# Optimization experiments

Measured on AMD Instinct MI355X. Metric: run time of the kernel, lower is better.

The kernel has to match this reference:

```python
import jax, jax.numpy as jnp
import numpy as np

INF = 1e38  # matches torch module's INF = 1e+38


def setup_inputs() -> dict:
    key = jax.random.key(0)
    k1, k2, k3 = jax.random.split(key, 3)
    n_len, batch, dim = 2048, 4, 512
    # scale query so QK^T logits don't fully saturate the softmax
    query = jax.random.normal(k1, (n_len, batch, dim), dtype=jnp.float32) * 0.05
    W_in = jax.random.normal(k2, (dim, dim), dtype=jnp.float32) * (1.0 / np.sqrt(dim))
    W_out = jax.random.normal(k3, (dim, 2 * dim), dtype=jnp.float32) * (1.0 / np.sqrt(2 * dim))
    return {"query": query, "W_in": W_in, "W_out": W_out}


def reference(query, W_in, W_out):
    # query: [n_len, batch, dim]; torch .t() swaps first two dims -> [batch, n_len, dim]
    q = jnp.transpose(query, (1, 0, 2))
    b, n, d = q.shape
    # attention_type == 'general': linear_in (no bias), y = x @ W^T
    q = jnp.einsum('bnd,ed->bne', q, W_in)
    # scores: [b, n, n]
    scores = jnp.einsum('bnd,bmd->bnm', q, q)
    # mask = triu(ones) INCLUDING diagonal -> set to -INF (row 0 fully masked)
    mask = jnp.triu(jnp.ones((n, n), dtype=bool))
    scores = jnp.where(mask[None, :, :], -INF, scores)
    weights = jax.nn.softmax(scores, axis=-1)  # row 0 becomes uniform (all -INF)
    # manual zero-out of row 0 of the attention weights
    weights = weights.at[:, 0, :].set(0.0)
    mix = jnp.einsum('bnm,bmd->bnd', weights, q)
    combined = jnp.concatenate([mix, q], axis=-1)  # [b, n, 2d]
    out = jnp.einsum('bnk,dk->bnd', combined, W_out)  # linear_out, no bias
    out = jax.nn.selu(out)
    # final .t() -> [n_len, batch, dim]
    return jnp.transpose(out, (1, 0, 2)), weights
```

## Files before the change

### kernel.cpp

```cpp
#include <hip/hip_runtime.h>
#include <hip/hip_bf16.h>

typedef unsigned short u16;
typedef unsigned int u32;

#define BATCH 4
#define NLEN 2048
#define DIM 512
#define LDSK 40
#define LDSB 72

typedef __attribute__((ext_vector_type(8))) __bf16 bf16x8;
typedef __attribute__((ext_vector_type(4))) float f32x4;

__device__ __forceinline__ u16 f32_to_bf16(float f) {
  union { float f; u32 u; } v; v.f = f;
  u32 u = v.u;
  return (u16)((u + 0x7FFFu + ((u >> 16) & 1u)) >> 16);
}
__device__ __forceinline__ u32 pk2(float lo, float hi) {
  return (u32)f32_to_bf16(lo) | ((u32)f32_to_bf16(hi) << 16);
}
__device__ __forceinline__ void stage8_f32(u16* dst, const float* src) {
  float4 a = *(const float4*)src;
  float4 b = *(const float4*)(src + 4);
  uint4 o;
  o.x = pk2(a.x, a.y); o.y = pk2(a.z, a.w);
  o.z = pk2(b.x, b.y); o.w = pk2(b.z, b.w);
  *(uint4*)dst = o;
}
__device__ __forceinline__ void stage16_f32(u16* dst, const float* src) {
  stage8_f32(dst, src); stage8_f32(dst + 8, src + 8);
}
__device__ __forceinline__ void stage8_bf16(u16* dst, const u16* src) {
  *(uint4*)dst = *(const uint4*)src;
}
__device__ __forceinline__ void stage16_bf16(u16* dst, const u16* src) {
  *(uint4*)dst = *(const uint4*)src;
  *(uint4*)(dst + 8) = *(const uint4*)(src + 8);
}

template <int MR, int NR>
__device__ __forceinline__ void mma_tile(const u16* As, const u16* Bs, f32x4 acc[MR][NR],
                                         int wm, int wn, int lr, int lk) {
  bf16x8 af[MR], bfr[NR];
#pragma unroll
  for (int m = 0; m < MR; ++m)
    af[m] = *(const bf16x8*)(As + (wm + m * 16 + lr) * LDSK + lk);
#pragma unroll
  for (int n = 0; n < NR; ++n)
    bfr[n] = *(const bf16x8*)(Bs + (wn + n * 16 + lr) * LDSK + lk);
#pragma unroll
  for (int m = 0; m < MR; ++m)
#pragma unroll
    for (int n = 0; n < NR; ++n)
      acc[m][n] = __builtin_amdgcn_mfma_f32_16x16x32_bf16(af[m], bfr[n], acc[m][n], 0, 0, 0);
}

__global__ __launch_bounds__(256) void k_qproj(const float* __restrict__ query,
                                               const float* __restrict__ W_in,
                                               u16* __restrict__ qp, u16* __restrict__ qt) {
  __shared__ u16 As[64 * LDSK];
  __shared__ u16 Bs[128 * LDSK];
  __shared__ u16 tbuf[128][72];
  const int t = threadIdx.x;
  const int lane = t & 63, wid = t >> 6;
  const int wm = (wid >> 1) * 32, wn = (wid & 1) * 64;
  const int lr = lane & 15, lk = (lane >> 4) * 8;
  const int trow4 = t >> 2, tseg = (t & 3) * 8;
  const int trow2 = t >> 1, thalf = (t & 1) * 16;
  const int rbase = blockIdx.y * 64;
  const int cbase = blockIdx.x * 128;
  const int rg = rbase + trow4;
  const int bb = rg >> 11, nn = rg & 2047;
  const float* aRow = query + (size_t)(nn * BATCH + bb) * DIM + tseg;
  const float* bRow = W_in + (size_t)(cbase + trow2) * DIM + thalf;
  f32x4 acc[2][4] = {};
  for (int k0 = 0; k0 < DIM; k0 += 32) {
    stage8_f32(As + trow4 * LDSK + tseg, aRow + k0);
    stage16_f32(Bs + trow2 * LDSK + thalf, bRow + k0);
    __syncthreads();
    mma_tile<2, 4>(As, Bs, acc, wm, wn, lr, lk);
    __syncthreads();
  }
#pragma unroll
  for (int m = 0; m < 2; ++m)
#pragma unroll
    for (int n = 0; n < 4; ++n)
#pragma unroll
      for (int j = 0; j < 4; ++j) {
        int rl = wm + m * 16 + (lane >> 4) * 4 + j;
        int cl = wn + n * 16 + lr;
        u16 v = f32_to_bf16(acc[m][n][j]);
        qp[(size_t)(rbase + rl) * DIM + cbase + cl] = v;
        tbuf[cl][rl] = v;
      }
  __syncthreads();
  const int bb0 = rbase >> 11, nbase = rbase & 2047;
#pragma unroll
  for (int i = 0; i < 4; ++i) {
    int idx = t + i * 256;
    int dl = idx >> 3, c = idx & 7;
    uint4 v = *(const uint4*)&tbuf[dl][c * 8];
    *(uint4*)(qt + (size_t)(bb0 * DIM + cbase + dl) * NLEN + nbase + c * 8) = v;
  }
}

__global__ __launch_bounds__(256) void k_scores(const u16* __restrict__ qp,
                                                u16* __restrict__ swf) {
  const int mt = blockIdx.x;
  const int nt = blockIdx.y;
  const int b = blockIdx.z;
  if (mt > (nt >> 1)) return;
  __shared__ u16 As[64 * LDSK];
  __shared__ u16 Bs[128 * LDSK];
  const int t = threadIdx.x;
  const int lane = t & 63, wid = t >> 6;
  const int wm = (wid >> 1) * 32, wn = (wid & 1) * 64;
  const int lr = lane & 15, lk = (lane >> 4) * 8;
  const int trow4 = t >> 2, tseg = (t & 3) * 8;
  const int trow2 = t >> 1, thalf = (t & 1) * 16;
  const u16* aRow = qp + (size_t)(b * NLEN + nt * 64 + trow4) * DIM + tseg;
  const u16* bRow = qp + (size_t)(b * NLEN + mt * 128 + trow2) * DIM + thalf;
  f32x4 acc[2][4] = {};
  for (int k0 = 0; k0 < DIM; k0 += 32) {
    stage8_bf16(As + trow4 * LDSK + tseg, aRow + k0);
    stage16_bf16(Bs + trow2 * LDSK + thalf, bRow + k0);
    __syncthreads();
    mma_tile<2, 4>(As, Bs, acc, wm, wn, lr, lk);
    __syncthreads();
  }
  const int NT = nt >> 1;
  u16* wtile = swf + ((size_t)(b * 136 + NT * (NT + 1) / 2 + mt) << 14);
  const int rowoff = (nt & 1) * 64;
#pragma unroll
  for (int m = 0; m < 2; ++m)
#pragma unroll
    for (int n = 0; n < 4; ++n)
#pragma unroll
      for (int j = 0; j < 4; ++j) {
        int rl = wm + m * 16 + (lane >> 4) * 4 + j;
        int cl = wn + n * 16 + lr;
        wtile[(rowoff + rl) * 128 + cl] = f32_to_bf16(acc[m][n][j]);
      }
}

__global__ __launch_bounds__(256) void k_softmax(u16* __restrict__ swf, float* __restrict__ w,
                                                 const float* __restrict__ W_out,
                                                 u16* __restrict__ wob) {
  const int n = blockIdx.x, b = blockIdx.y;
  const int t = threadIdx.x;
  if (n >= NLEN) {
    int g = ((n - NLEN) * 4 + b) * 256 + t;
#pragma unroll
    for (int i = 0; i < 4; ++i) {
      int e = g * 32 + i * 8;
      stage8_f32(wob + e, W_out + e);
    }
    return;
  }
  float* wrow = w + ((size_t)b * NLEN + n) * NLEN;
  const int nt = n >> 7;
  const size_t tb = ((size_t)(b * 136 + nt * (nt + 1) / 2) << 14) + ((size_t)(n & 127) << 7);
  __shared__ float srow[NLEN];
  __shared__ float red[4];
  if (n == 0) {
    for (int i = t; i < NLEN / 4; i += 256) ((float4*)wrow)[i] = float4{0, 0, 0, 0};
    if (t < 16) ((uint4*)(swf + tb))[t] = uint4{0, 0, 0, 0};
    return;
  }
  const int lane = t & 63, wid = t >> 6;
  const int nchunk = (nt + 1) * 16;
  float mx = -1e38f;
  for (int idx = t; idx < nchunk; idx += 256) {
    const int mt = idx >> 4, c = idx & 15;
    uint4 rv = *(const uint4*)(swf + tb + ((size_t)mt << 14) + c * 8);
    int m0 = mt * 128 + c * 8;
    u32 wds[4] = {rv.x, rv.y, rv.z, rv.w};
#pragma unroll
    for (int wi = 0; wi < 4; ++wi) {
      float v0 = __uint_as_float(wds[wi] << 16);
      float v1 = __uint_as_float(wds[wi] & 0xffff0000u);
      int m = m0 + wi * 2;
      srow[m] = v0; srow[m + 1] = v1;
      if (m < n) mx = fmaxf(mx, v0);
      if (m + 1 < n) mx = fmaxf(mx, v1);
    }
  }
#pragma unroll
  for (int off = 32; off; off >>= 1) mx = fmaxf(mx, __shfl_xor(mx, off));
  if (lane == 0) red[wid] = mx;
  __syncthreads();
  mx = fmaxf(fmaxf(red[0], red[1]), fmaxf(red[2], red[3]));
  float sum = 0.f;
  for (int m = t; m < n; m += 256) {
    float e = __expf(srow[m] - mx);
    srow[m] = e;
    sum += e;
  }
#pragma unroll
  for (int off = 32; off; off >>= 1) sum += __shfl_xor(sum, off);
  __syncthreads();
  if (lane == 0) red[wid] = sum;
  __syncthreads();
  float inv = 1.0f / (red[0] + red[1] + red[2] + red[3]);
  {
    int m0 = t * 8;
    float vals[8];
#pragma unroll
    for (int e = 0; e < 8; ++e) { int m = m0 + e; vals[e] = (m < n) ? srow[m] * inv : 0.f; }
    ((float4*)wrow)[t * 2] = float4{vals[0], vals[1], vals[2], vals[3]};
    ((float4*)wrow)[t * 2 + 1] = float4{vals[4], vals[5], vals[6], vals[7]};
  }
  for (int idx = t; idx < nchunk; idx += 256) {
    const int mt = idx >> 4, c = idx & 15;
    int m0 = mt * 128 + c * 8;
    u32 wo[4];
#pragma unroll
    for (int wi = 0; wi < 4; ++wi) {
      int m = m0 + wi * 2;
      float v0 = (m < n) ? srow[m] * inv : 0.f;
      float v1 = (m + 1 < n) ? srow[m + 1] * inv : 0.f;
      wo[wi] = (u32)f32_to_bf16(v0) | ((u32)f32_to_bf16(v1) << 16);
    }
    *(uint4*)(swf + tb + ((size_t)mt << 14) + c * 8) = uint4{wo[0], wo[1], wo[2], wo[3]};
  }
}

template <int ROWS>
__device__ __forceinline__ void mix_body(u16* As, u16* Bs,
                                         const u16* __restrict__ swf,
                                         const u16* __restrict__ qt,
                                         u16* __restrict__ amix,
                                         int b, int dt, int nt, int seg) {
  constexpr int MR = (ROWS == 128) ? 4 : 2;
  constexpr int NR = 4;
  const int t = threadIdx.x;
  const int lane = t & 63, wid = t >> 6;
  const int wm = (wid >> 1) * (ROWS / 2), wn = (wid & 1) * 64;
  const int lr = lane & 15, lk = (lane >> 4) * 8;
  const int trow2 = t >> 1, thalf = (t & 1) * 16;
  const int ar = (ROWS == 128) ? (t >> 1) : (t >> 2);
  const int ac = (ROWS == 128) ? ((t & 1) * 16) : ((t & 3) * 8);
  const size_t tribase = (size_t)(b * 136 + nt * (nt + 1) / 2) << 14;
  const int rowloc = seg * ROWS;
  const u16* bRow = qt + (size_t)(b * DIM + dt * 128 + trow2) * NLEN + thalf;
  f32x4 acc[MR][NR] = {};
  const int nsteps = (nt + 1) * 4;
  for (int kstep = 0; kstep < nsteps; ++kstep) {
    const int k0 = kstep * 32;
    const int mt = k0 >> 7;
    const u16* aSrc = swf + tribase + ((size_t)mt << 14) + (rowloc + ar) * 128 + (k0 & 127) + ac;
    if (ROWS == 128) stage16_bf16(As + ar * LDSK + ac, aSrc);
    else stage8_bf16(As + ar * LDSK + ac, aSrc);
    stage16_bf16(Bs + trow2 * LDSK + thalf, bRow + k0);
    __syncthreads();
    mma_tile<MR, NR>(As, Bs, acc, wm, wn, lr, lk);
    __syncthreads();
  }
#pragma unroll
  for (int m = 0; m < MR; ++m)
#pragma unroll
    for (int n = 0; n < NR; ++n)
#pragma unroll
      for (int j2 = 0; j2 < 4; ++j2) {
        int row = nt * 128 + rowloc + wm + m * 16 + (lane >> 4) * 4 + j2;
        int col = dt * 128 + wn + n * 16 + lr;
        amix[(size_t)(b * NLEN + row) * DIM + col] = f32_to_bf16(acc[m][n][j2]);
      }
}

__global__ __launch_bounds__(256) void k_mix(const u16* __restrict__ swf,
                                             const u16* __restrict__ qt,
                                             u16* __restrict__ amix) {
  __shared__ u16 As[128 * LDSK];
  __shared__ u16 Bs[128 * LDSK];
  const int bid = blockIdx.x;
  const int j = bid >> 4;
  const int bdt = bid & 15;
  const int b = bdt >> 2, dt = bdt & 3;
  if (j < 24) {
    const int nt = 15 - (j >> 1), seg = j & 1;
    mix_body<64>(As, Bs, swf, qt, amix, b, dt, nt, seg);
  } else {
    const int nt = 27 - j;
    mix_body<128>(As, Bs, swf, qt, amix, b, dt, nt, 0);
  }
}

__global__ __launch_bounds__(256) void k_out(const u16* __restrict__ amix,
                                             const u16* __restrict__ qp,
                                             const u16* __restrict__ wob,
                                             float* __restrict__ out) {
  __shared__ u16 As[128 * LDSB];
  __shared__ u16 Bs[64 * LDSB];
  const int et = blockIdx.x;
  const int rt = blockIdx.y;
  const int t = threadIdx.x;
  const int lane = t & 63, wid = t >> 6;
  const int wm = (wid >> 1) * 64, wn = (wid & 1) * 32;
  const int lr = lane & 15, lk = (lane >> 4) * 8;
  const int rbase = rt * 128;
  const int ar = t >> 3, ac = (t & 7) * 8;
  const int br = t >> 2, bc = (t & 3) * 16;
  const u16* aMix = amix + (size_t)rbase * DIM;
  const u16* aQ = qp + (size_t)rbase * DIM;
  const u16* bW = wob + (size_t)(et * 64 + br) * (2 * DIM) + bc;
  f32x4 acc[4][2] = {};
  for (int k0 = 0; k0 < 2 * DIM; k0 += 64) {
    const u16* asrc = (k0 < DIM) ? (aMix + k0) : (aQ + (k0 - DIM));
#pragma unroll
    for (int i = 0; i < 4; ++i)
      *(uint4*)(As + (ar + i * 32) * LDSB + ac) =
          *(const uint4*)(asrc + (size_t)(ar + i * 32) * DIM + ac);
    *(uint4*)(Bs + br * LDSB + bc) = *(const uint4*)(bW + k0);
    *(uint4*)(Bs + br * LDSB + bc + 8) = *(const uint4*)(bW + k0 + 8);
    __syncthreads();
#pragma unroll
    for (int kk = 0; kk < 64; kk += 32) {
      bf16x8 af[4], bfr[2];
#pragma unroll
      for (int m = 0; m < 4; ++m)
        af[m] = *(const bf16x8*)(As + (wm + m * 16 + lr) * LDSB + kk + lk);
#pragma unroll
      for (int n = 0; n < 2; ++n)
        bfr[n] = *(const bf16x8*)(Bs + (wn + n * 16 + lr) * LDSB + kk + lk);
#pragma unroll
      for (int m = 0; m < 4; ++m)
#pragma unroll
        for (int n = 0; n < 2; ++n)
          acc[m][n] = __builtin_amdgcn_mfma_f32_16x16x32_bf16(af[m], bfr[n], acc[m][n], 0, 0, 0);
    }
    __syncthreads();
  }
  const float sc = 1.0507009873554805f;
  const float al = 1.6732632423543772f;
#pragma unroll
  for (int m = 0; m < 4; ++m)
#pragma unroll
    for (int n = 0; n < 2; ++n)
#pragma unroll
      for (int j = 0; j < 4; ++j) {
        int row = rbase + wm + m * 16 + (lane >> 4) * 4 + j;
        int col = et * 64 + wn + n * 16 + lr;
        int b2 = row >> 11, n2 = row & 2047;
        float v = acc[m][n][j];
        v = (v > 0.f) ? sc * v : sc * al * (__expf(v) - 1.f);
        out[(size_t)(n2 * BATCH + b2) * DIM + col] = v;
      }
}

extern "C" void kernel_launch(void* const* d_in, const int* in_sizes, int n_in,
                              void* d_out, int out_size, void* d_ws, size_t ws_size,
                              hipStream_t stream) {
  const float* query = (const float*)d_in[0];
  const float* W_in = (const float*)d_in[1];
  const float* W_out = (const float*)d_in[2];
  float* out0 = (float*)d_out;
  float* w = out0 + (size_t)NLEN * BATCH * DIM;

  const size_t PSZ = (size_t)BATCH * NLEN * DIM;
  u16* qp = (u16*)d_ws;
  u16* qt = qp + PSZ;
  u16* amix = qt + PSZ;
  u16* swf = amix + PSZ;
  u16* wob = swf + (size_t)BATCH * 136 * 16384;

  dim3 blk(256);
  k_qproj<<<dim3(DIM / 128, (BATCH * NLEN) / 64), blk, 0, stream>>>(query, W_in, qp, qt);
  k_scores<<<dim3(16, 32, BATCH), blk, 0, stream>>>(qp, swf);
  k_softmax<<<dim3(NLEN + 16, BATCH), blk, 0, stream>>>(swf, w, W_out, wob);
  k_mix<<<dim3(448), blk, 0, stream>>>(swf, qt, amix);
  k_out<<<dim3(8, 64), blk, 0, stream>>>(amix, qp, wob, out0);
}
```

Measured before the change: 140.2 us.

## Use direct global-to-LDS loads, larger tiles, and split-K mix with fold kernel

The scores, mix and output GEMMs now stage tiles through global_load_lds straight into unpadded 64-wide LDS rows instead of going through registers. Scores use 128x128 tiles with a compact triangular grid, so no blocks exit early. The mix kernel drops the 64-row half-tiles in favour of 128-row tiles, and for long rows splits K into two partial sums that a new k_fold kernel adds in bf16. The intent is to cut register staging and per-block overhead and to balance work across blocks, at the cost of an extra launch, an extra workspace buffer, a double bf16 rounding of the split rows, and possible LDS bank conflicts from the unpadded layout.

Measured after the change: 124.5 us, median of 2. 1.13x faster.

```diff
diff --git a/kernel.cpp b/kernel.cpp
--- a/kernel.cpp
+++ b/kernel.cpp
@@ -8,10 +8,12 @@
 #define NLEN 2048
 #define DIM 512
 #define LDSK 40
-#define LDSB 72
 
 typedef __attribute__((ext_vector_type(8))) __bf16 bf16x8;
 typedef __attribute__((ext_vector_type(4))) float f32x4;
+
+typedef const __attribute__((address_space(1))) void gv_t;
+typedef __attribute__((address_space(3))) void lv_t;
 
 __device__ __forceinline__ u16 f32_to_bf16(float f) {
   union { float f; u32 u; } v; v.f = f;
@@ -32,29 +34,23 @@
 __device__ __forceinline__ void stage16_f32(u16* dst, const float* src) {
   stage8_f32(dst, src); stage8_f32(dst + 8, src + 8);
 }
-__device__ __forceinline__ void stage8_bf16(u16* dst, const u16* src) {
-  *(uint4*)dst = *(const uint4*)src;
-}
-__device__ __forceinline__ void stage16_bf16(u16* dst, const u16* src) {
-  *(uint4*)dst = *(const uint4*)src;
-  *(uint4*)(dst + 8) = *(const uint4*)(src + 8);
-}
-
-template <int MR, int NR>
-__device__ __forceinline__ void mma_tile(const u16* As, const u16* Bs, f32x4 acc[MR][NR],
-                                         int wm, int wn, int lr, int lk) {
-  bf16x8 af[MR], bfr[NR];
-#pragma unroll
-  for (int m = 0; m < MR; ++m)
-    af[m] = *(const bf16x8*)(As + (wm + m * 16 + lr) * LDSK + lk);
-#pragma unroll
-  for (int n = 0; n < NR; ++n)
-    bfr[n] = *(const bf16x8*)(Bs + (wn + n * 16 + lr) * LDSK + lk);
-#pragma unroll
-  for (int m = 0; m < MR; ++m)
-#pragma unroll
-    for (int n = 0; n < NR; ++n)
-      acc[m][n] = __builtin_amdgcn_mfma_f32_16x16x32_bf16(af[m], bfr[n], acc[m][n], 0, 0, 0);
+__device__ __forceinline__ u32 addpk_bf16(u32 a, u32 b) {
+  float a0 = __uint_as_float(a << 16), a1 = __uint_as_float(a & 0xffff0000u);
+  float b0 = __uint_as_float(b << 16), b1 = __uint_as_float(b & 0xffff0000u);
+  return pk2(a0 + b0, a1 + b1);
+}
+
+template <int NRPW>
+__device__ __forceinline__ void glds_rows(const u16* gsrc, size_t gstride, u16* lds,
+                                          int wrow0, int lane) {
+  const int r = lane >> 3;
+  const int c = (lane & 7) * 8;
+#pragma unroll
+  for (int i = 0; i < NRPW; i += 8) {
+    const int row = wrow0 + i + r;
+    __builtin_amdgcn_global_load_lds((gv_t*)(gsrc + (size_t)row * gstride + c),
+                                     (lv_t*)(lds + row * 64 + c), 16, 0, 0);
+  }
 }
 
 __global__ __launch_bounds__(256) void k_qproj(const float* __restrict__ query,
@@ -80,7 +76,16 @@
     stage8_f32(As + trow4 * LDSK + tseg, aRow + k0);
     stage16_f32(Bs + trow2 * LDSK + thalf, bRow + k0);
     __syncthreads();
-    mma_tile<2, 4>(As, Bs, acc, wm, wn, lr, lk);
+    bf16x8 af[2], bfr[4];
+#pragma unroll
+    for (int m = 0; m < 2; ++m) af[m] = *(const bf16x8*)(As + (wm + m * 16 + lr) * LDSK + lk);
+#pragma unroll
+    for (int n = 0; n < 4; ++n) bfr[n] = *(const bf16x8*)(Bs + (wn + n * 16 + lr) * LDSK + lk);
+#pragma unroll
+    for (int m = 0; m < 2; ++m)
+#pragma unroll
+      for (int n = 0; n < 4; ++n)
+        acc[m][n] = __builtin_amdgcn_mfma_f32_16x16x32_bf16(af[m], bfr[n], acc[m][n], 0, 0, 0);
     __syncthreads();
   }
 #pragma unroll
@@ -108,40 +113,49 @@
 
 __global__ __launch_bounds__(256) void k_scores(const u16* __restrict__ qp,
                                                 u16* __restrict__ swf) {
-  const int mt = blockIdx.x;
-  const int nt = blockIdx.y;
-  const int b = blockIdx.z;
-  if (mt > (nt >> 1)) return;
-  __shared__ u16 As[64 * LDSK];
-  __shared__ u16 Bs[128 * LDSK];
-  const int t = threadIdx.x;
-  const int lane = t & 63, wid = t >> 6;
-  const int wm = (wid >> 1) * 32, wn = (wid & 1) * 64;
+  const int tri = blockIdx.x;
+  const int b = blockIdx.y;
+  int nt = 0, cacc = 0;
+  while (cacc + nt + 1 <= tri) { cacc += nt + 1; ++nt; }
+  const int mt = tri - cacc;
+  __shared__ u16 As[128 * 64];
+  __shared__ u16 Bs[128 * 64];
+  const int t = threadIdx.x;
+  const int lane = t & 63, wid = t >> 6;
+  const int wm = (wid >> 1) * 64, wn = (wid & 1) * 64;
   const int lr = lane & 15, lk = (lane >> 4) * 8;
-  const int trow4 = t >> 2, tseg = (t & 3) * 8;
-  const int trow2 = t >> 1, thalf = (t & 1) * 16;
-  const u16* aRow = qp + (size_t)(b * NLEN + nt * 64 + trow4) * DIM + tseg;
-  const u16* bRow = qp + (size_t)(b * NLEN + mt * 128 + trow2) * DIM + thalf;
-  f32x4 acc[2][4] = {};
-  for (int k0 = 0; k0 < DIM; k0 += 32) {
-    stage8_bf16(As + trow4 * LDSK + tseg, aRow + k0);
-    stage16_bf16(Bs + trow2 * LDSK + thalf, bRow + k0);
-    __syncthreads();
-    mma_tile<2, 4>(As, Bs, acc, wm, wn, lr, lk);
-    __syncthreads();
-  }
-  const int NT = nt >> 1;
-  u16* wtile = swf + ((size_t)(b * 136 + NT * (NT + 1) / 2 + mt) << 14);
-  const int rowoff = (nt & 1) * 64;
-#pragma unroll
-  for (int m = 0; m < 2; ++m)
+  const u16* ag = qp + (size_t)(b * NLEN + nt * 128) * DIM;
+  const u16* bg = qp + (size_t)(b * NLEN + mt * 128) * DIM;
+  f32x4 acc[4][4] = {};
+  for (int k0 = 0; k0 < DIM; k0 += 64) {
+    glds_rows<32>(ag + k0, DIM, As, wid * 32, lane);
+    glds_rows<32>(bg + k0, DIM, Bs, wid * 32, lane);
+    __syncthreads();
+#pragma unroll
+    for (int kk = 0; kk < 64; kk += 32) {
+      bf16x8 af[4], bfr[4];
+#pragma unroll
+      for (int m = 0; m < 4; ++m) af[m] = *(const bf16x8*)(As + (wm + m * 16 + lr) * 64 + kk + lk);
+#pragma unroll
+      for (int n = 0; n < 4; ++n) bfr[n] = *(const bf16x8*)(Bs + (wn + n * 16 + lr) * 64 + kk + lk);
+#pragma unroll
+      for (int m = 0; m < 4; ++m)
+#pragma unroll
+        for (int n = 0; n < 4; ++n)
+          acc[m][n] = __builtin_amdgcn_mfma_f32_16x16x32_bf16(af[m], bfr[n], acc[m][n], 0, 0, 0);
+    }
+    __syncthreads();
+  }
+  u16* wtile = swf + ((size_t)(b * 136 + tri) << 14);
+#pragma unroll
+  for (int m = 0; m < 4; ++m)
 #pragma unroll
     for (int n = 0; n < 4; ++n)
 #pragma unroll
       for (int j = 0; j < 4; ++j) {
         int rl = wm + m * 16 + (lane >> 4) * 4 + j;
         int cl = wn + n * 16 + lr;
-        wtile[(rowoff + rl) * 128 + cl] = f32_to_bf16(acc[m][n][j]);
+        wtile[rl * 128 + cl] = f32_to_bf16(acc[m][n][j]);
       }
 }
 
@@ -227,64 +241,78 @@
   }
 }
 
-template <int ROWS>
-__device__ __forceinline__ void mix_body(u16* As, u16* Bs,
-                                         const u16* __restrict__ swf,
-                                         const u16* __restrict__ qt,
-                                         u16* __restrict__ amix,
-                                         int b, int dt, int nt, int seg) {
-  constexpr int MR = (ROWS == 128) ? 4 : 2;
-  constexpr int NR = 4;
-  const int t = threadIdx.x;
-  const int lane = t & 63, wid = t >> 6;
-  const int wm = (wid >> 1) * (ROWS / 2), wn = (wid & 1) * 64;
-  const int lr = lane & 15, lk = (lane >> 4) * 8;
-  const int trow2 = t >> 1, thalf = (t & 1) * 16;
-  const int ar = (ROWS == 128) ? (t >> 1) : (t >> 2);
-  const int ac = (ROWS == 128) ? ((t & 1) * 16) : ((t & 3) * 8);
-  const size_t tribase = (size_t)(b * 136 + nt * (nt + 1) / 2) << 14;
-  const int rowloc = seg * ROWS;
-  const u16* bRow = qt + (size_t)(b * DIM + dt * 128 + trow2) * NLEN + thalf;
-  f32x4 acc[MR][NR] = {};
-  const int nsteps = (nt + 1) * 4;
-  for (int kstep = 0; kstep < nsteps; ++kstep) {
-    const int k0 = kstep * 32;
-    const int mt = k0 >> 7;
-    const u16* aSrc = swf + tribase + ((size_t)mt << 14) + (rowloc + ar) * 128 + (k0 & 127) + ac;
-    if (ROWS == 128) stage16_bf16(As + ar * LDSK + ac, aSrc);
-    else stage8_bf16(As + ar * LDSK + ac, aSrc);
-    stage16_bf16(Bs + trow2 * LDSK + thalf, bRow + k0);
-    __syncthreads();
-    mma_tile<MR, NR>(As, Bs, acc, wm, wn, lr, lk);
-    __syncthreads();
-  }
-#pragma unroll
-  for (int m = 0; m < MR; ++m)
-#pragma unroll
-    for (int n = 0; n < NR; ++n)
-#pragma unroll
-      for (int j2 = 0; j2 < 4; ++j2) {
-        int row = nt * 128 + rowloc + wm + m * 16 + (lane >> 4) * 4 + j2;
-        int col = dt * 128 + wn + n * 16 + lr;
-        amix[(size_t)(b * NLEN + row) * DIM + col] = f32_to_bf16(acc[m][n][j2]);
-      }
-}
-
 __global__ __launch_bounds__(256) void k_mix(const u16* __restrict__ swf,
                                              const u16* __restrict__ qt,
-                                             u16* __restrict__ amix) {
-  __shared__ u16 As[128 * LDSK];
-  __shared__ u16 Bs[128 * LDSK];
-  const int bid = blockIdx.x;
-  const int j = bid >> 4;
-  const int bdt = bid & 15;
+                                             u16* __restrict__ amix,
+                                             u16* __restrict__ mix1) {
+  const int j = blockIdx.x >> 4;
+  const int bdt = blockIdx.x & 15;
   const int b = bdt >> 2, dt = bdt & 3;
-  if (j < 24) {
-    const int nt = 15 - (j >> 1), seg = j & 1;
-    mix_body<64>(As, Bs, swf, qt, amix, b, dt, nt, seg);
+  int nt, kt0, ktn, slot;
+  if (j < 16) {
+    nt = 15 - (j >> 1);
+    if ((j & 1) == 0) { kt0 = 0; ktn = 8; slot = 0; }
+    else { kt0 = 8; ktn = nt + 1; slot = 1; }
   } else {
-    const int nt = 27 - j;
-    mix_body<128>(As, Bs, swf, qt, amix, b, dt, nt, 0);
+    nt = 23 - j; kt0 = 0; ktn = nt + 1; slot = 0;
+  }
+  __shared__ u16 As[128 * 64];
+  __shared__ u16 Bs[128 * 64];
+  const int t = threadIdx.x;
+  const int lane = t & 63, wid = t >> 6;
+  const int wm = (wid >> 1) * 64, wn = (wid & 1) * 64;
+  const int lr = lane & 15, lk = (lane >> 4) * 8;
+  const size_t tribase = (size_t)(b * 136 + nt * (nt + 1) / 2) << 14;
+  const u16* bgbase = qt + (size_t)(b * DIM + dt * 128) * NLEN;
+  f32x4 acc[4][4] = {};
+  for (int ks = kt0 * 2; ks < ktn * 2; ++ks) {
+    const u16* ag = swf + tribase + ((size_t)(ks >> 1) << 14) + (ks & 1) * 64;
+    glds_rows<32>(ag, 128, As, wid * 32, lane);
+    glds_rows<32>(bgbase + ks * 64, NLEN, Bs, wid * 32, lane);
+    __syncthreads();
+#pragma unroll
+    for (int kk = 0; kk < 64; kk += 32) {
+      bf16x8 af[4], bfr[4];
+#pragma unroll
+      for (int m = 0; m < 4; ++m) af[m] = *(const bf16x8*)(As + (wm + m * 16 + lr) * 64 + kk + lk);
+#pragma unroll
+      for (int n = 0; n < 4; ++n) bfr[n] = *(const bf16x8*)(Bs + (wn + n * 16 + lr) * 64 + kk + lk);
+#pragma unroll
+      for (int m = 0; m < 4; ++m)
+#pragma unroll
+        for (int n = 0; n < 4; ++n)
+          acc[m][n] = __builtin_amdgcn_mfma_f32_16x16x32_bf16(af[m], bfr[n], acc[m][n], 0, 0, 0);
+    }
+    __syncthreads();
+  }
+  u16* dst = slot ? mix1 : amix;
+#pragma unroll
+  for (int m = 0; m < 4; ++m)
+#pragma unroll
+    for (int n = 0; n < 4; ++n)
+#pragma unroll
+      for (int j2 = 0; j2 < 4; ++j2) {
+        int row = nt * 128 + wm + m * 16 + (lane >> 4) * 4 + j2;
+        int col = dt * 128 + wn + n * 16 + lr;
+        dst[(size_t)(b * NLEN + row) * DIM + col] = f32_to_bf16(acc[m][n][j2]);
+      }
+}
+
+__global__ __launch_bounds__(256) void k_fold(u16* __restrict__ amix,
+                                              const u16* __restrict__ mix1) {
+  const int t = threadIdx.x;
+#pragma unroll
+  for (int i = 0; i < 2; ++i) {
+    int g = (blockIdx.x * 2 + i) * 256 + t;
+    int rowlin = g >> 6, within = g & 63;
+    int b = rowlin >> 10, n = 1024 + (rowlin & 1023);
+    size_t off = ((size_t)(b * NLEN + n) * DIM) + within * 8;
+    uint4 a = *(const uint4*)(amix + off);
+    uint4 c = *(const uint4*)(mix1 + off);
+    uint4 o;
+    o.x = addpk_bf16(a.x, c.x); o.y = addpk_bf16(a.y, c.y);
+    o.z = addpk_bf16(a.z, c.z); o.w = addpk_bf16(a.w, c.w);
+    *(uint4*)(amix + off) = o;
   }
 }
 
@@ -292,8 +320,8 @@
                                              const u16* __restrict__ qp,
                                              const u16* __restrict__ wob,
                                              float* __restrict__ out) {
-  __shared__ u16 As[128 * LDSB];
-  __shared__ u16 Bs[64 * LDSB];
+  __shared__ u16 As[128 * 64];
+  __shared__ u16 Bs[64 * 64];
   const int et = blockIdx.x;
   const int rt = blockIdx.y;
   const int t = threadIdx.x;
@@ -301,30 +329,22 @@
   const int wm = (wid >> 1) * 64, wn = (wid & 1) * 32;
   const int lr = lane & 15, lk = (lane >> 4) * 8;
   const int rbase = rt * 128;
-  const int ar = t >> 3, ac = (t & 7) * 8;
-  const int br = t >> 2, bc = (t & 3) * 16;
   const u16* aMix = amix + (size_t)rbase * DIM;
   const u16* aQ = qp + (size_t)rbase * DIM;
-  const u16* bW = wob + (size_t)(et * 64 + br) * (2 * DIM) + bc;
+  const u16* bW = wob + (size_t)(et * 64) * (2 * DIM);
   f32x4 acc[4][2] = {};
   for (int k0 = 0; k0 < 2 * DIM; k0 += 64) {
-    const u16* asrc = (k0 < DIM) ? (aMix + k0) : (aQ + (k0 - DIM));
-#pragma unroll
-    for (int i = 0; i < 4; ++i)
-      *(uint4*)(As + (ar + i * 32) * LDSB + ac) =
-          *(const uint4*)(asrc + (size_t)(ar + i * 32) * DIM + ac);
-    *(uint4*)(Bs + br * LDSB + bc) = *(const uint4*)(bW + k0);
-    *(uint4*)(Bs + br * LDSB + bc + 8) = *(const uint4*)(bW + k0 + 8);
+    const u16* ag = (k0 < DIM) ? (aMix + k0) : (aQ + (k0 - DIM));
+    glds_rows<32>(ag, DIM, As, wid * 32, lane);
+    glds_rows<16>(bW + k0, 2 * DIM, Bs, wid * 16, lane);
     __syncthreads();
 #pragma unroll
     for (int kk = 0; kk < 64; kk += 32) {
       bf16x8 af[4], bfr[2];
 #pragma unroll
-      for (int m = 0; m < 4; ++m)
-        af[m] = *(const bf16x8*)(As + (wm + m * 16 + lr) * LDSB + kk + lk);
-#pragma unroll
-      for (int n = 0; n < 2; ++n)
-        bfr[n] = *(const bf16x8*)(Bs + (wn + n * 16 + lr) * LDSB + kk + lk);
+      for (int m = 0; m < 4; ++m) af[m] = *(const bf16x8*)(As + (wm + m * 16 + lr) * 64 + kk + lk);
+#pragma unroll
+      for (int n = 0; n < 2; ++n) bfr[n] = *(const bf16x8*)(Bs + (wn + n * 16 + lr) * 64 + kk + lk);
 #pragma unroll
       for (int m = 0; m < 4; ++m)
 #pragma unroll
@@ -363,13 +383,15 @@
   u16* qp = (u16*)d_ws;
   u16* qt = qp + PSZ;
   u16* amix = qt + PSZ;
-  u16* swf = amix + PSZ;
+  u16* mix1 = amix + PSZ;
+  u16* swf = mix1 + PSZ;
   u16* wob = swf + (size_t)BATCH * 136 * 16384;
 
   dim3 blk(256);
   k_qproj<<<dim3(DIM / 128, (BATCH * NLEN) / 64), blk, 0, stream>>>(query, W_in, qp, qt);
-  k_scores<<<dim3(16, 32, BATCH), blk, 0, stream>>>(qp, swf);
+  k_scores<<<dim3(136, BATCH), blk, 0, stream>>>(qp, swf);
   k_softmax<<<dim3(NLEN + 16, BATCH), blk, 0, stream>>>(swf, w, W_out, wob);
-  k_mix<<<dim3(448), blk, 0, stream>>>(swf, qt, amix);
+  k_mix<<<dim3(384), blk, 0, stream>>>(swf, qt, amix, mix1);
+  k_fold<<<dim3(512), blk, 0, stream>>>(amix, mix1);
   k_out<<<dim3(8, 64), blk, 0, stream>>>(amix, qp, wob, out0);
 }
```
